# Performance work log

Measured on AMD Instinct MI355X. Metric: run time of the kernel, lower is better.

Reference implementation:

```python
import jax, jax.numpy as jnp
import numpy as np

NUM_HEADS = 8  # matches init_kwargs

def setup_inputs() -> dict:
    key = jax.random.key(0)
    ks = jax.random.split(key, 5)
    b, n, c = 8, 4096, 512
    scale_in = 1.0 / np.sqrt(c)
    return {
        'x': jax.random.normal(ks[0], (b, n, c), jnp.float32),
        'wqkv_w': jax.random.normal(ks[1], (3 * c, c), jnp.float32) * scale_in,
        'wqkv_b': jax.random.normal(ks[2], (3 * c,), jnp.float32) * 0.02,
        'wp_w': jax.random.normal(ks[3], (c, c), jnp.float32) * scale_in,
        'wp_b': jax.random.normal(ks[4], (c,), jnp.float32) * 0.02,
    }

def reference(x, wqkv_w, wqkv_b, wp_w, wp_b):
    b, n, c = x.shape
    h = NUM_HEADS
    d = c // h
    # QKV projection (torch Linear: x @ W^T + b)
    qkv = x @ wqkv_w.T + wqkv_b                      # (b, n, 3c)
    qkv = jnp.transpose(qkv.reshape(b, n, 3, c), (2, 0, 1, 3))
    q, k, v = qkv[0], qkv[1], qkv[2]                 # each (b, n, c)
    # Faithful to original: reshape (b,n,h,d) -> (b,h,n,d) is a FLAT
    # reinterpretation (torch .reshape), not a transpose.
    q = q.reshape(b, n, h, d).reshape(b, h, n, d)
    k = k.reshape(b, n, h, d).reshape(b, h, n, d)
    v = v.reshape(b, n, h, d).reshape(b, h, n, d)
    # Channel (cross-covariance) attention: contract over tokens n.
    scores = jnp.einsum('bhnd,bhne->bhde', q, k) / jnp.sqrt(jnp.float32(d))
    weights = jax.nn.softmax(scores, axis=-1)        # softmax over head_dim
    y = jnp.einsum('bhde,bhme->bhdm', weights, v)    # (b, h, d, n)
    y = jnp.transpose(y, (0, 3, 1, 2)).reshape(b, n, c)
    return y @ wp_w.T + wp_b
```

## Files before the change

kernel.cpp:

```cpp
#include <hip/hip_runtime.h>

typedef short s16x8 __attribute__((ext_vector_type(8)));
typedef float f32x4 __attribute__((ext_vector_type(4)));
typedef unsigned short us;

__device__ inline us f2bf(float f){
    union{float f;unsigned u;} v{f};
    unsigned r = v.u + 0x7fff + ((v.u>>16)&1);
    return (us)(r>>16);
}

__device__ __forceinline__ void glds16(const us* g, us* l){
    __builtin_amdgcn_global_load_lds(
        (const __attribute__((address_space(1))) unsigned int*)(g),
        (__attribute__((address_space(3))) unsigned int*)(l), 16, 0, 0);
}

__global__ void cast_all(const float* __restrict__ x, const float* __restrict__ wqkv_w,
                         const float* __restrict__ wp_w, us* __restrict__ xbf,
                         us* __restrict__ wqkvbf, us* __restrict__ wpbf){
    int i = blockIdx.x*blockDim.x + threadIdx.x;
    const float* s; us* d; int j;
    if(i < 4194304){ s = x; d = xbf; j = i; }
    else if(i < 4390912){ s = wqkv_w; d = wqkvbf; j = i - 4194304; }
    else { s = wp_w; d = wpbf; j = i - 4390912; }
    float4 f = ((const float4*)s)[j];
    ushort4 o;
    o.x = f2bf(f.x); o.y = f2bf(f.y); o.z = f2bf(f.z); o.w = f2bf(f.w);
    ((ushort4*)d)[j] = o;
}

__launch_bounds__(256,4)
__global__ void gemm_qkv(const us* __restrict__ A, const us* __restrict__ B,
                         const float* __restrict__ bias, us* __restrict__ C){
    __shared__ __attribute__((aligned(16))) us sA[128*64];
    __shared__ __attribute__((aligned(16))) us sB[128*64];
    int t = threadIdx.x;
    int id = blockIdx.x;
    int xcd = id & 7, s = id >> 3;
    int nt = s % 12, mt = xcd*32 + s/12;
    int lane = t&63, wave = t>>6, quad = lane>>4, l15 = lane&15;
    int wm = wave>>1, wn = wave&1;

    int l8 = lane>>3;
    int sw = ((lane&7) ^ l8)*8;
    const us* Ag = A + (size_t)(mt*128 + wave*32 + l8)*512 + sw;
    const us* Bg = B + (size_t)(nt*128 + wave*32 + l8)*512 + sw;
    us* sAw = &sA[(wave*32)*64];
    us* sBw = &sB[(wave*32)*64];

    f32x4 acc[4][4];
    #pragma unroll
    for(int i=0;i<4;i++)
        #pragma unroll
        for(int j=0;j<4;j++) acc[i][j] = (f32x4){0.f,0.f,0.f,0.f};

    for(int k0=0; k0<512; k0+=64){
        glds16(Ag + k0,           sAw);
        glds16(Ag + 8*512 + k0,   sAw + 8*64);
        glds16(Ag + 16*512 + k0,  sAw + 16*64);
        glds16(Ag + 24*512 + k0,  sAw + 24*64);
        glds16(Bg + k0,           sBw);
        glds16(Bg + 8*512 + k0,   sBw + 8*64);
        glds16(Bg + 16*512 + k0,  sBw + 16*64);
        glds16(Bg + 24*512 + k0,  sBw + 24*64);
        __syncthreads();
        #pragma unroll
        for(int ks=0; ks<2; ks++){
            int kc = ks*4 + quad;
            s16x8 af[4], bfr[4];
            #pragma unroll
            for(int i=0;i<4;i++){
                int r = wm*64 + i*16 + l15;
                af[i] = *(const s16x8*)&sA[r*64 + ((kc ^ (r&7))<<3)];
            }
            #pragma unroll
            for(int j=0;j<4;j++){
                int r = wn*64 + j*16 + l15;
                bfr[j] = *(const s16x8*)&sB[r*64 + ((kc ^ (r&7))<<3)];
            }
            #pragma unroll
            for(int i=0;i<4;i++)
                #pragma unroll
                for(int j=0;j<4;j++)
                    acc[i][j] = __builtin_amdgcn_mfma_f32_16x16x32_bf16(af[i], bfr[j], acc[i][j], 0,0,0);
        }
        __syncthreads();
    }

    int row0 = mt*128 + wm*64, col0 = nt*128 + wn*64;
    #pragma unroll
    for(int j=0;j<4;j++){
        int col = col0 + j*16 + l15;
        float bv = bias[col];
        #pragma unroll
        for(int i=0;i<4;i++){
            int rbase = row0 + i*16 + quad*4;
            #pragma unroll
            for(int r=0;r<4;r++)
                C[(size_t)(rbase+r)*1536 + col] = f2bf(acc[i][j][r] + bv);
        }
    }
}

__launch_bounds__(256,4)
__global__ void attn_scores_mfma(const us* __restrict__ qkv, float* __restrict__ Sp){
    __shared__ __attribute__((aligned(16))) us sQt[64*72];
    __shared__ __attribute__((aligned(16))) us sKt[64*72];
    int t = threadIdx.x;
    int kb = blockIdx.x, head = blockIdx.y;
    int lane = t & 63, w = t >> 6;
    int quad = lane >> 4, l15 = lane & 15;
    int p = t & 31;
    int d0 = (t >> 5) * 8;

    f32x4 acc[4];
    #pragma unroll
    for(int j=0;j<4;j++) acc[j] = (f32x4){0.f,0.f,0.f,0.f};

    for(int chunk=0; chunk<8; chunk++){
        int r0 = head*512 + kb*64 + chunk*8;
        const us* g = qkv + (size_t)(r0 + (p>>2))*1536 + (2*(p&3))*64 + d0;
        union{uint4 v; us h[8];} q0, q1, k0, k1;
        q0.v = *(const uint4*)g;         q1.v = *(const uint4*)(g + 64);
        k0.v = *(const uint4*)(g + 512); k1.v = *(const uint4*)(g + 576);
        #pragma unroll
        for(int j=0;j<8;j++){
            *(unsigned*)&sQt[(d0+j)*72 + 2*p] = (unsigned)q0.h[j] | ((unsigned)q1.h[j]<<16);
            *(unsigned*)&sKt[(d0+j)*72 + 2*p] = (unsigned)k0.h[j] | ((unsigned)k1.h[j]<<16);
        }
        __syncthreads();
        int d = w*16 + l15;
        #pragma unroll
        for(int ks=0; ks<2; ks++){
            int tb = ks*4 + quad;
            s16x8 af = *(const s16x8*)&sQt[d*72 + tb*8];
            #pragma unroll
            for(int jt=0; jt<4; jt++){
                int e = jt*16 + l15;
                s16x8 bfv = *(const s16x8*)&sKt[e*72 + tb*8];
                acc[jt] = __builtin_amdgcn_mfma_f32_16x16x32_bf16(af, bfv, acc[jt], 0,0,0);
            }
        }
        __syncthreads();
    }

    float* S = Sp + (size_t)(kb*64 + head)*4096;
    #pragma unroll
    for(int jt=0; jt<4; jt++){
        int e = jt*16 + l15;
        #pragma unroll
        for(int r=0; r<4; r++){
            int d = w*16 + quad*4 + r;
            S[d*64 + e] = acc[jt][r];
        }
    }
}

__global__ void softmax64(const float* __restrict__ Sp, us* __restrict__ W){
    int head = blockIdx.x>>2, part = blockIdx.x&3;
    int t = threadIdx.x;
    int d = part*16 + (t>>4), e0 = (t&15)*4;
    float4 v = {0.f,0.f,0.f,0.f};
    for(int kb=0; kb<8; kb++){
        float4 f = *(const float4*)&Sp[(size_t)(kb*64 + head)*4096 + d*64 + e0];
        v.x+=f.x; v.y+=f.y; v.z+=f.z; v.w+=f.w;
    }
    v.x*=0.125f; v.y*=0.125f; v.z*=0.125f; v.w*=0.125f;
    float m = fmaxf(fmaxf(v.x,v.y), fmaxf(v.z,v.w));
    m = fmaxf(m, __shfl_xor(m, 1));
    m = fmaxf(m, __shfl_xor(m, 2));
    m = fmaxf(m, __shfl_xor(m, 4));
    m = fmaxf(m, __shfl_xor(m, 8));
    v.x=__expf(v.x-m); v.y=__expf(v.y-m); v.z=__expf(v.z-m); v.w=__expf(v.w-m);
    float s = v.x+v.y+v.z+v.w;
    s += __shfl_xor(s, 1);
    s += __shfl_xor(s, 2);
    s += __shfl_xor(s, 4);
    s += __shfl_xor(s, 8);
    float inv = 1.f/s;
    union{uint2 u; us h[4];} o;
    o.h[0]=f2bf(v.x*inv); o.h[1]=f2bf(v.y*inv); o.h[2]=f2bf(v.z*inv); o.h[3]=f2bf(v.w*inv);
    *(uint2*)&W[(size_t)head*4096 + d*64 + e0] = o.u;
}

__launch_bounds__(256,2)
__global__ void fold(const us* __restrict__ Wsm, const us* __restrict__ wpbf,
                     us* __restrict__ Mcat){
    __shared__ us sWt[64*72];
    int t = threadIdx.x;
    int head = blockIdx.x>>2, part = blockIdx.x&3;
    int b = head>>3, h = head&7;
    int lane = t&63, w = t>>6, quad = lane>>4, l15 = lane&15;
    #pragma unroll
    for(int it=0; it<2; it++){
        int idx = it*2048 + t*8;
        int d = idx>>6, e0 = idx&63;
        union{uint4 v; us s[8];} q;
        q.v = *(const uint4*)&Wsm[(size_t)head*4096 + idx];
        #pragma unroll
        for(int j=0;j<8;j++) sWt[(e0+j)*72 + d] = q.s[j];
    }
    __syncthreads();
    #pragma unroll
    for(int i=0;i<2;i++){
        int nO = part*128 + w*32 + i*16 + l15;
        s16x8 af0 = *(const s16x8*)&wpbf[(size_t)nO*512 + h*64 + quad*8];
        s16x8 af1 = *(const s16x8*)&wpbf[(size_t)nO*512 + h*64 + 32 + quad*8];
        #pragma unroll
        for(int j=0;j<4;j++){
            s16x8 bf0 = *(const s16x8*)&sWt[(j*16+l15)*72 + quad*8];
            s16x8 bf1 = *(const s16x8*)&sWt[(j*16+l15)*72 + 32 + quad*8];
            f32x4 acc = (f32x4){0.f,0.f,0.f,0.f};
            acc = __builtin_amdgcn_mfma_f32_16x16x32_bf16(af0, bf0, acc, 0,0,0);
            acc = __builtin_amdgcn_mfma_f32_16x16x32_bf16(af1, bf1, acc, 0,0,0);
            #pragma unroll
            for(int r=0;r<4;r++){
                int row = part*128 + w*32 + i*16 + quad*4 + r;
                Mcat[((size_t)(b*512 + row))*512 + h*64 + j*16 + l15] = f2bf(acc[r]);
            }
        }
    }
}

__launch_bounds__(256,4)
__global__ void gemm_vout(const us* __restrict__ qkv, const us* __restrict__ Mcat,
                          const float* __restrict__ bias, float* __restrict__ out){
    __shared__ __attribute__((aligned(16))) us sA[128*64];
    __shared__ __attribute__((aligned(16))) us sB[128*64];
    int t = threadIdx.x;
    int id = blockIdx.x;
    int xcd = id & 7, s = id >> 3;
    int nt = s & 3, mt = xcd*32 + (s>>2);
    int b = mt>>5, mr = mt&31;
    int lane = t&63, wave = t>>6, quad = lane>>4, l15 = lane&15;
    int wm = wave>>1, wn = wave&1;

    int l8 = lane>>3;
    int sw = ((lane&7) ^ l8)*8;
    const us* Abase = qkv + ((size_t)(8*b)*512 + mr*16 + wave*4)*1536 + 1024 + l8*64 + sw;
    const us* Bbase = Mcat + ((size_t)(b*512 + nt*128 + wave*32 + l8))*512 + sw;
    us* sAw = &sA[(wave*32)*64];
    us* sBw = &sB[(wave*32)*64];

    f32x4 acc[4][4];
    #pragma unroll
    for(int i=0;i<4;i++)
        #pragma unroll
        for(int j=0;j<4;j++) acc[i][j] = (f32x4){0.f,0.f,0.f,0.f};

    for(int h=0; h<8; h++){
        const us* Ah = Abase + (size_t)h*512*1536;
        const us* Bh = Bbase + h*64;
        glds16(Ah,           sAw);
        glds16(Ah + 1536,    sAw + 8*64);
        glds16(Ah + 2*1536,  sAw + 16*64);
        glds16(Ah + 3*1536,  sAw + 24*64);
        glds16(Bh,           sBw);
        glds16(Bh + 8*512,   sBw + 8*64);
        glds16(Bh + 16*512,  sBw + 16*64);
        glds16(Bh + 24*512,  sBw + 24*64);
        __syncthreads();
        #pragma unroll
        for(int ks=0; ks<2; ks++){
            int kc = ks*4 + quad;
            s16x8 af[4], bfr[4];
            #pragma unroll
            for(int i=0;i<4;i++){
                int r = wm*64 + i*16 + l15;
                af[i] = *(const s16x8*)&sA[r*64 + ((kc ^ (r&7))<<3)];
            }
            #pragma unroll
            for(int j=0;j<4;j++){
                int r = wn*64 + j*16 + l15;
                bfr[j] = *(const s16x8*)&sB[r*64 + ((kc ^ (r&7))<<3)];
            }
            #pragma unroll
            for(int i=0;i<4;i++)
                #pragma unroll
                for(int j=0;j<4;j++)
                    acc[i][j] = __builtin_amdgcn_mfma_f32_16x16x32_bf16(af[i], bfr[j], acc[i][j], 0,0,0);
        }
        __syncthreads();
    }

    int row0 = b*4096 + mr*128 + wm*64;
    int col0 = nt*128 + wn*64;
    #pragma unroll
    for(int j=0;j<4;j++){
        int col = col0 + j*16 + l15;
        float bv = bias[col];
        #pragma unroll
        for(int i=0;i<4;i++){
            int rbase = row0 + i*16 + quad*4;
            #pragma unroll
            for(int r2=0;r2<4;r2++)
                out[(size_t)(rbase+r2)*512 + col] = acc[i][j][r2] + bv;
        }
    }
}

extern "C" void kernel_launch(void* const* d_in, const int* in_sizes, int n_in,
                              void* d_out, int out_size, void* d_ws, size_t ws_size,
                              hipStream_t stream){
    const float* x      = (const float*)d_in[0];
    const float* wqkv_w = (const float*)d_in[1];
    const float* wqkv_b = (const float*)d_in[2];
    const float* wp_w   = (const float*)d_in[3];
    const float* wp_b   = (const float*)d_in[4];

    char* ws = (char*)d_ws;
    us*    qkvbf  = (us*)(ws);
    us*    xbf    = (us*)(ws + 100663296);
    float* Spart  = (float*)(ws + 134217728);
    us*    Wsm    = (us*)(ws + 142606336);
    us*    Mcat   = (us*)(ws + 143130624);
    us*    wqkvbf = (us*)(ws + 147324928);
    us*    wpbf   = (us*)(ws + 148897792);

    cast_all<<<17408,256,0,stream>>>(x, wqkv_w, wp_w, xbf, wqkvbf, wpbf);

    gemm_qkv<<<3072,256,0,stream>>>(xbf, wqkvbf, wqkv_b, qkvbf);

    attn_scores_mfma<<<dim3(8,64),256,0,stream>>>(qkvbf, Spart);
    softmax64<<<256,256,0,stream>>>(Spart, Wsm);
    fold<<<256,256,0,stream>>>(Wsm, wpbf, Mcat);

    gemm_vout<<<1024,256,0,stream>>>(qkvbf, Mcat, wp_b, (float*)d_out);
}
```

Baseline: 233.3 us.

## Double-buffer GEMMs with 256x256 tiles, 8 waves, and MFMA priority scheduling

```diff
diff --git a/kernel.cpp b/kernel.cpp
--- a/kernel.cpp
+++ b/kernel.cpp
@@ -30,75 +30,103 @@
     ((ushort4*)d)[j] = o;
 }
 
-__launch_bounds__(256,4)
+__launch_bounds__(512,2)
 __global__ void gemm_qkv(const us* __restrict__ A, const us* __restrict__ B,
                          const float* __restrict__ bias, us* __restrict__ C){
-    __shared__ __attribute__((aligned(16))) us sA[128*64];
-    __shared__ __attribute__((aligned(16))) us sB[128*64];
+    __shared__ __attribute__((aligned(16))) us sA[2][16384];
+    __shared__ __attribute__((aligned(16))) us sB[2][16384];
     int t = threadIdx.x;
     int id = blockIdx.x;
     int xcd = id & 7, s = id >> 3;
-    int nt = s % 12, mt = xcd*32 + s/12;
+    int nt = s % 6, mt = xcd*16 + s/6;
     int lane = t&63, wave = t>>6, quad = lane>>4, l15 = lane&15;
-    int wm = wave>>1, wn = wave&1;
-
+    int wm = wave>>2, wn = wave&3;
     int l8 = lane>>3;
     int sw = ((lane&7) ^ l8)*8;
-    const us* Ag = A + (size_t)(mt*128 + wave*32 + l8)*512 + sw;
-    const us* Bg = B + (size_t)(nt*128 + wave*32 + l8)*512 + sw;
-    us* sAw = &sA[(wave*32)*64];
-    us* sBw = &sB[(wave*32)*64];
-
-    f32x4 acc[4][4];
-    #pragma unroll
-    for(int i=0;i<4;i++)
-        #pragma unroll
-        for(int j=0;j<4;j++) acc[i][j] = (f32x4){0.f,0.f,0.f,0.f};
-
-    for(int k0=0; k0<512; k0+=64){
-        glds16(Ag + k0,           sAw);
-        glds16(Ag + 8*512 + k0,   sAw + 8*64);
-        glds16(Ag + 16*512 + k0,  sAw + 16*64);
-        glds16(Ag + 24*512 + k0,  sAw + 24*64);
-        glds16(Bg + k0,           sBw);
-        glds16(Bg + 8*512 + k0,   sBw + 8*64);
-        glds16(Bg + 16*512 + k0,  sBw + 16*64);
-        glds16(Bg + 24*512 + k0,  sBw + 24*64);
-        __syncthreads();
-        #pragma unroll
-        for(int ks=0; ks<2; ks++){
-            int kc = ks*4 + quad;
-            s16x8 af[4], bfr[4];
-            #pragma unroll
-            for(int i=0;i<4;i++){
-                int r = wm*64 + i*16 + l15;
-                af[i] = *(const s16x8*)&sA[r*64 + ((kc ^ (r&7))<<3)];
-            }
-            #pragma unroll
-            for(int j=0;j<4;j++){
-                int r = wn*64 + j*16 + l15;
-                bfr[j] = *(const s16x8*)&sB[r*64 + ((kc ^ (r&7))<<3)];
-            }
-            #pragma unroll
-            for(int i=0;i<4;i++)
+
+    const us* Ag = A + (size_t)(mt*256 + wave*8 + l8)*512 + sw;
+    const us* Bg = B + (size_t)(nt*256 + wave*8 + l8)*512 + sw;
+    us* sA0 = &sA[0][0];
+    us* sB0 = &sB[0][0];
+    int wofs = wave*512;
+
+    f32x4 acc[8][4];
+    #pragma unroll
+    for(int m=0;m<8;m++)
+        #pragma unroll
+        for(int n=0;n<4;n++) acc[m][n] = (f32x4){0.f,0.f,0.f,0.f};
+
+    #pragma unroll
+    for(int r=0;r<4;r++) glds16(Ag + r*32768, sA0 + wofs + r*4096);
+    #pragma unroll
+    for(int r=0;r<4;r++) glds16(Bg + r*32768, sB0 + wofs + r*4096);
+    asm volatile("s_waitcnt vmcnt(0)" ::: "memory");
+    __builtin_amdgcn_s_barrier();
+
+    for(int kt=0; kt<8; ++kt){
+        int cur = kt & 1;
+        const us* sAc = sA0 + cur*16384;
+        const us* sBc = sB0 + cur*16384;
+        if(kt < 7){
+            int kn = (kt+1)*64;
+            int nx = (cur^1)*16384 + wofs;
+            #pragma unroll
+            for(int r=0;r<4;r++) glds16(Ag + r*32768 + kn, sA0 + nx + r*4096);
+            #pragma unroll
+            for(int r=0;r<4;r++) glds16(Bg + r*32768 + kn, sB0 + nx + r*4096);
+        }
+        s16x8 bfr[4][2];
+        #pragma unroll
+        for(int n=0;n<4;n++){
+            int rw = wn*64 + n*16 + l15;
+            #pragma unroll
+            for(int ks=0;ks<2;ks++){
+                int kc = ks*4 + quad;
+                bfr[n][ks] = *(const s16x8*)&sBc[rw*64 + ((kc ^ (rw&7))<<3)];
+            }
+        }
+        #pragma unroll
+        for(int p=0;p<4;p++){
+            s16x8 af[2][2];
+            #pragma unroll
+            for(int i=0;i<2;i++){
+                int rw = wm*128 + (2*p+i)*16 + l15;
                 #pragma unroll
-                for(int j=0;j<4;j++)
-                    acc[i][j] = __builtin_amdgcn_mfma_f32_16x16x32_bf16(af[i], bfr[j], acc[i][j], 0,0,0);
-        }
-        __syncthreads();
-    }
-
-    int row0 = mt*128 + wm*64, col0 = nt*128 + wn*64;
-    #pragma unroll
-    for(int j=0;j<4;j++){
-        int col = col0 + j*16 + l15;
+                for(int ks=0;ks<2;ks++){
+                    int kc = ks*4 + quad;
+                    af[i][ks] = *(const s16x8*)&sAc[rw*64 + ((kc ^ (rw&7))<<3)];
+                }
+            }
+            __builtin_amdgcn_s_barrier();
+            __builtin_amdgcn_s_setprio(1);
+            #pragma unroll
+            for(int ks=0;ks<2;ks++)
+                #pragma unroll
+                for(int i=0;i<2;i++)
+                    #pragma unroll
+                    for(int n=0;n<4;n++)
+                        acc[2*p+i][n] = __builtin_amdgcn_mfma_f32_16x16x32_bf16(
+                                            af[i][ks], bfr[n][ks], acc[2*p+i][n], 0,0,0);
+            __builtin_amdgcn_s_setprio(0);
+            __builtin_amdgcn_s_barrier();
+        }
+        if(kt < 7){
+            asm volatile("s_waitcnt vmcnt(0)" ::: "memory");
+            __builtin_amdgcn_s_barrier();
+        }
+    }
+
+    int row0 = mt*256 + wm*128, col0 = nt*256 + wn*64;
+    #pragma unroll
+    for(int n=0;n<4;n++){
+        int col = col0 + n*16 + l15;
         float bv = bias[col];
         #pragma unroll
-        for(int i=0;i<4;i++){
-            int rbase = row0 + i*16 + quad*4;
+        for(int m=0;m<8;m++){
+            int rb = row0 + m*16 + quad*4;
             #pragma unroll
             for(int r=0;r<4;r++)
-                C[(size_t)(rbase+r)*1536 + col] = f2bf(acc[i][j][r] + bv);
+                C[(size_t)(rb+r)*1536 + col] = f2bf(acc[m][n][r] + bv);
         }
     }
 }
@@ -223,79 +251,106 @@
     }
 }
 
-__launch_bounds__(256,4)
+__launch_bounds__(512,2)
 __global__ void gemm_vout(const us* __restrict__ qkv, const us* __restrict__ Mcat,
                           const float* __restrict__ bias, float* __restrict__ out){
-    __shared__ __attribute__((aligned(16))) us sA[128*64];
-    __shared__ __attribute__((aligned(16))) us sB[128*64];
+    __shared__ __attribute__((aligned(16))) us sA[2][16384];
+    __shared__ __attribute__((aligned(16))) us sB[2][16384];
     int t = threadIdx.x;
     int id = blockIdx.x;
     int xcd = id & 7, s = id >> 3;
-    int nt = s & 3, mt = xcd*32 + (s>>2);
-    int b = mt>>5, mr = mt&31;
+    int f = xcd*32 + s;
+    int b = f>>5, rr = f&31, mtb = rr>>1, nt = rr&1;
     int lane = t&63, wave = t>>6, quad = lane>>4, l15 = lane&15;
-    int wm = wave>>1, wn = wave&1;
-
+    int wm = wave>>2, wn = wave&3;
     int l8 = lane>>3;
     int sw = ((lane&7) ^ l8)*8;
-    const us* Abase = qkv + ((size_t)(8*b)*512 + mr*16 + wave*4)*1536 + 1024 + l8*64 + sw;
-    const us* Bbase = Mcat + ((size_t)(b*512 + nt*128 + wave*32 + l8))*512 + sw;
-    us* sAw = &sA[(wave*32)*64];
-    us* sBw = &sB[(wave*32)*64];
-
-    f32x4 acc[4][4];
-    #pragma unroll
-    for(int i=0;i<4;i++)
-        #pragma unroll
-        for(int j=0;j<4;j++) acc[i][j] = (f32x4){0.f,0.f,0.f,0.f};
-
-    for(int h=0; h<8; h++){
-        const us* Ah = Abase + (size_t)h*512*1536;
-        const us* Bh = Bbase + h*64;
-        glds16(Ah,           sAw);
-        glds16(Ah + 1536,    sAw + 8*64);
-        glds16(Ah + 2*1536,  sAw + 16*64);
-        glds16(Ah + 3*1536,  sAw + 24*64);
-        glds16(Bh,           sBw);
-        glds16(Bh + 8*512,   sBw + 8*64);
-        glds16(Bh + 16*512,  sBw + 16*64);
-        glds16(Bh + 24*512,  sBw + 24*64);
-        __syncthreads();
-        #pragma unroll
-        for(int ks=0; ks<2; ks++){
-            int kc = ks*4 + quad;
-            s16x8 af[4], bfr[4];
-            #pragma unroll
-            for(int i=0;i<4;i++){
-                int r = wm*64 + i*16 + l15;
-                af[i] = *(const s16x8*)&sA[r*64 + ((kc ^ (r&7))<<3)];
-            }
-            #pragma unroll
-            for(int j=0;j<4;j++){
-                int r = wn*64 + j*16 + l15;
-                bfr[j] = *(const s16x8*)&sB[r*64 + ((kc ^ (r&7))<<3)];
-            }
-            #pragma unroll
-            for(int i=0;i<4;i++)
+
+    const us* Ag = qkv + (size_t)(b*4096 + mtb*32 + wave)*1536 + 1024 + l8*64 + sw;
+    const us* Bg = Mcat + (size_t)(b*512 + nt*256 + wave*8 + l8)*512 + sw;
+    us* sA0 = &sA[0][0];
+    us* sB0 = &sB[0][0];
+    int wofs = wave*512;
+
+    f32x4 acc[8][4];
+    #pragma unroll
+    for(int m=0;m<8;m++)
+        #pragma unroll
+        for(int n=0;n<4;n++) acc[m][n] = (f32x4){0.f,0.f,0.f,0.f};
+
+    #pragma unroll
+    for(int r=0;r<4;r++) glds16(Ag + r*12288, sA0 + wofs + r*4096);
+    #pragma unroll
+    for(int r=0;r<4;r++) glds16(Bg + r*32768, sB0 + wofs + r*4096);
+    asm volatile("s_waitcnt vmcnt(0)" ::: "memory");
+    __builtin_amdgcn_s_barrier();
+
+    for(int kt=0; kt<8; ++kt){
+        int cur = kt & 1;
+        const us* sAc = sA0 + cur*16384;
+        const us* sBc = sB0 + cur*16384;
+        if(kt < 7){
+            int nx = (cur^1)*16384 + wofs;
+            size_t ka = (size_t)(kt+1)*786432;
+            int kb2 = (kt+1)*64;
+            #pragma unroll
+            for(int r=0;r<4;r++) glds16(Ag + ka + r*12288, sA0 + nx + r*4096);
+            #pragma unroll
+            for(int r=0;r<4;r++) glds16(Bg + kb2 + r*32768, sB0 + nx + r*4096);
+        }
+        s16x8 bfr[4][2];
+        #pragma unroll
+        for(int n=0;n<4;n++){
+            int rw = wn*64 + n*16 + l15;
+            #pragma unroll
+            for(int ks=0;ks<2;ks++){
+                int kc = ks*4 + quad;
+                bfr[n][ks] = *(const s16x8*)&sBc[rw*64 + ((kc ^ (rw&7))<<3)];
+            }
+        }
+        #pragma unroll
+        for(int p=0;p<4;p++){
+            s16x8 af[2][2];
+            #pragma unroll
+            for(int i=0;i<2;i++){
+                int rw = wm*128 + (2*p+i)*16 + l15;
                 #pragma unroll
-                for(int j=0;j<4;j++)
-                    acc[i][j] = __builtin_amdgcn_mfma_f32_16x16x32_bf16(af[i], bfr[j], acc[i][j], 0,0,0);
-        }
-        __syncthreads();
-    }
-
-    int row0 = b*4096 + mr*128 + wm*64;
-    int col0 = nt*128 + wn*64;
-    #pragma unroll
-    for(int j=0;j<4;j++){
-        int col = col0 + j*16 + l15;
+                for(int ks=0;ks<2;ks++){
+                    int kc = ks*4 + quad;
+                    af[i][ks] = *(const s16x8*)&sAc[rw*64 + ((kc ^ (rw&7))<<3)];
+                }
+            }
+            __builtin_amdgcn_s_barrier();
+            __builtin_amdgcn_s_setprio(1);
+            #pragma unroll
+            for(int ks=0;ks<2;ks++)
+                #pragma unroll
+                for(int i=0;i<2;i++)
+                    #pragma unroll
+                    for(int n=0;n<4;n++)
+                        acc[2*p+i][n] = __builtin_amdgcn_mfma_f32_16x16x32_bf16(
+                                            af[i][ks], bfr[n][ks], acc[2*p+i][n], 0,0,0);
+            __builtin_amdgcn_s_setprio(0);
+            __builtin_amdgcn_s_barrier();
+        }
+        if(kt < 7){
+            asm volatile("s_waitcnt vmcnt(0)" ::: "memory");
+            __builtin_amdgcn_s_barrier();
+        }
+    }
+
+    int row0 = b*4096 + mtb*256 + wm*128;
+    int col0 = nt*256 + wn*64;
+    #pragma unroll
+    for(int n=0;n<4;n++){
+        int col = col0 + n*16 + l15;
         float bv = bias[col];
         #pragma unroll
-        for(int i=0;i<4;i++){
-            int rbase = row0 + i*16 + quad*4;
+        for(int m=0;m<8;m++){
+            int rb = row0 + m*16 + quad*4;
             #pragma unroll
             for(int r2=0;r2<4;r2++)
-                out[(size_t)(rbase+r2)*512 + col] = acc[i][j][r2] + bv;
+                out[(size_t)(rb+r2)*512 + col] = acc[m][n][r2] + bv;
         }
     }
 }
@@ -320,11 +375,11 @@
 
     cast_all<<<17408,256,0,stream>>>(x, wqkv_w, wp_w, xbf, wqkvbf, wpbf);
 
-    gemm_qkv<<<3072,256,0,stream>>>(xbf, wqkvbf, wqkv_b, qkvbf);
+    gemm_qkv<<<768,512,0,stream>>>(xbf, wqkvbf, wqkv_b, qkvbf);
 
     attn_scores_mfma<<<dim3(8,64),256,0,stream>>>(qkvbf, Spart);
     softmax64<<<256,256,0,stream>>>(Spart, Wsm);
     fold<<<256,256,0,stream>>>(Wsm, wpbf, Mcat);
 
-    gemm_vout<<<1024,256,0,stream>>>(qkvbf, Mcat, wp_b, (float*)d_out);
-}
+    gemm_vout<<<256,512,0,stream>>>(qkvbf, Mcat, wp_b, (float*)d_out);
+}
```

New measurement: 262.6 us. 12.6% more time.

## Restructure QKV GEMM into 256x256 double-buffered tiles with interleaved prefetch

Applied to the files above, without the earlier changes.

```diff
diff --git a/kernel.cpp b/kernel.cpp
--- a/kernel.cpp
+++ b/kernel.cpp
@@ -30,75 +30,159 @@
     ((ushort4*)d)[j] = o;
 }
 
-__launch_bounds__(256,4)
+__launch_bounds__(512,2)
 __global__ void gemm_qkv(const us* __restrict__ A, const us* __restrict__ B,
                          const float* __restrict__ bias, us* __restrict__ C){
-    __shared__ __attribute__((aligned(16))) us sA[128*64];
-    __shared__ __attribute__((aligned(16))) us sB[128*64];
+    __shared__ __attribute__((aligned(16))) us sA[2][16384];
+    __shared__ __attribute__((aligned(16))) us sB[2][16384];
     int t = threadIdx.x;
     int id = blockIdx.x;
     int xcd = id & 7, s = id >> 3;
-    int nt = s % 12, mt = xcd*32 + s/12;
-    int lane = t&63, wave = t>>6, quad = lane>>4, l15 = lane&15;
-    int wm = wave>>1, wn = wave&1;
-
+    int nt = s % 6, mt = xcd*16 + s/6;
+    int lane = t&63, w = t>>6, quad = lane>>4, l15 = lane&15;
+    int wm = w>>2, wn = w&3;
     int l8 = lane>>3;
     int sw = ((lane&7) ^ l8)*8;
-    const us* Ag = A + (size_t)(mt*128 + wave*32 + l8)*512 + sw;
-    const us* Bg = B + (size_t)(nt*128 + wave*32 + l8)*512 + sw;
-    us* sAw = &sA[(wave*32)*64];
-    us* sBw = &sB[(wave*32)*64];
-
-    f32x4 acc[4][4];
-    #pragma unroll
-    for(int i=0;i<4;i++)
-        #pragma unroll
-        for(int j=0;j<4;j++) acc[i][j] = (f32x4){0.f,0.f,0.f,0.f};
-
-    for(int k0=0; k0<512; k0+=64){
-        glds16(Ag + k0,           sAw);
-        glds16(Ag + 8*512 + k0,   sAw + 8*64);
-        glds16(Ag + 16*512 + k0,  sAw + 16*64);
-        glds16(Ag + 24*512 + k0,  sAw + 24*64);
-        glds16(Bg + k0,           sBw);
-        glds16(Bg + 8*512 + k0,   sBw + 8*64);
-        glds16(Bg + 16*512 + k0,  sBw + 16*64);
-        glds16(Bg + 24*512 + k0,  sBw + 24*64);
-        __syncthreads();
-        #pragma unroll
-        for(int ks=0; ks<2; ks++){
-            int kc = ks*4 + quad;
-            s16x8 af[4], bfr[4];
-            #pragma unroll
-            for(int i=0;i<4;i++){
-                int r = wm*64 + i*16 + l15;
-                af[i] = *(const s16x8*)&sA[r*64 + ((kc ^ (r&7))<<3)];
-            }
-            #pragma unroll
-            for(int j=0;j<4;j++){
-                int r = wn*64 + j*16 + l15;
-                bfr[j] = *(const s16x8*)&sB[r*64 + ((kc ^ (r&7))<<3)];
-            }
+
+    int rA0 = wm*128 + (w&3)*8;
+    int rB0 = (w>>1)*64 + (w&1)*8;
+    const us* Ag = A + (size_t)(mt*256 + rA0 + l8)*512 + sw;
+    const us* Bg = B + (size_t)(nt*256 + rB0 + l8)*512 + sw;
+    us* sA0 = &sA[0][0];
+    us* sB0 = &sB[0][0];
+    int aofs = rA0*64, bofs = rB0*64;
+
+#define STA(r,kt,bo) glds16(Ag + (size_t)(r)*16384 + (size_t)(kt)*64, sA0 + (bo) + aofs + (r)*2048)
+#define STB(r,kt,bo) glds16(Bg + (size_t)(r)*8192  + (size_t)(kt)*64, sB0 + (bo) + bofs + (r)*1024)
+
+    f32x4 acc[8][4];
+    #pragma unroll
+    for(int m=0;m<8;m++)
+        #pragma unroll
+        for(int n=0;n<4;n++) acc[m][n] = (f32x4){0.f,0.f,0.f,0.f};
+
+    STA(0,0,0); STA(1,0,0); STB(0,0,0); STB(1,0,0);
+    STB(2,0,0); STB(3,0,0); STA(2,0,0); STA(3,0,0);
+    asm volatile("s_waitcnt vmcnt(4)" ::: "memory");
+    __builtin_amdgcn_s_barrier();
+
+    s16x8 aF[4][2], bF[4][2];
+    for(int kt=0; kt<8; ++kt){
+        int co = (kt&1)*16384, no = co^16384;
+        const us* sAc = sA0 + co;
+        const us* sBc = sB0 + co;
+
+        #pragma unroll
+        for(int i=0;i<4;i++){
+            int rw = wm*128 + i*16 + l15;
+            #pragma unroll
+            for(int ks=0;ks<2;ks++){
+                int kc = ks*4 + quad;
+                aF[i][ks] = *(const s16x8*)&sAc[rw*64 + ((kc ^ (rw&7))<<3)];
+            }
+        }
+        #pragma unroll
+        for(int n=0;n<2;n++){
+            int rw = wn*64 + n*16 + l15;
+            #pragma unroll
+            for(int ks=0;ks<2;ks++){
+                int kc = ks*4 + quad;
+                bF[n][ks] = *(const s16x8*)&sBc[rw*64 + ((kc ^ (rw&7))<<3)];
+            }
+        }
+        if(kt<7){ STA(0,kt+1,no); STA(1,kt+1,no);
+                  asm volatile("s_waitcnt vmcnt(4)" ::: "memory"); }
+        else    { asm volatile("s_waitcnt vmcnt(2)" ::: "memory"); }
+        __builtin_amdgcn_s_barrier();
+        __builtin_amdgcn_s_setprio(1);
+        #pragma unroll
+        for(int ks=0;ks<2;ks++)
             #pragma unroll
             for(int i=0;i<4;i++)
                 #pragma unroll
-                for(int j=0;j<4;j++)
-                    acc[i][j] = __builtin_amdgcn_mfma_f32_16x16x32_bf16(af[i], bfr[j], acc[i][j], 0,0,0);
-        }
-        __syncthreads();
-    }
-
-    int row0 = mt*128 + wm*64, col0 = nt*128 + wn*64;
-    #pragma unroll
-    for(int j=0;j<4;j++){
-        int col = col0 + j*16 + l15;
-        float bv = bias[col];
+                for(int n=0;n<2;n++)
+                    acc[i][n] = __builtin_amdgcn_mfma_f32_16x16x32_bf16(bF[n][ks], aF[i][ks], acc[i][n], 0,0,0);
+        __builtin_amdgcn_s_setprio(0);
+        __builtin_amdgcn_s_barrier();
+
+        #pragma unroll
+        for(int n=2;n<4;n++){
+            int rw = wn*64 + n*16 + l15;
+            #pragma unroll
+            for(int ks=0;ks<2;ks++){
+                int kc = ks*4 + quad;
+                bF[n][ks] = *(const s16x8*)&sBc[rw*64 + ((kc ^ (rw&7))<<3)];
+            }
+        }
+        if(kt<7){ STB(0,kt+1,no); STB(1,kt+1,no);
+                  asm volatile("s_waitcnt vmcnt(4)" ::: "memory"); }
+        else    { asm volatile("s_waitcnt vmcnt(0)" ::: "memory"); }
+        __builtin_amdgcn_s_barrier();
+        __builtin_amdgcn_s_setprio(1);
+        #pragma unroll
+        for(int ks=0;ks<2;ks++)
+            #pragma unroll
+            for(int i=0;i<4;i++)
+                #pragma unroll
+                for(int n=2;n<4;n++)
+                    acc[i][n] = __builtin_amdgcn_mfma_f32_16x16x32_bf16(bF[n][ks], aF[i][ks], acc[i][n], 0,0,0);
+        __builtin_amdgcn_s_setprio(0);
+        __builtin_amdgcn_s_barrier();
+
         #pragma unroll
         for(int i=0;i<4;i++){
-            int rbase = row0 + i*16 + quad*4;
-            #pragma unroll
-            for(int r=0;r<4;r++)
-                C[(size_t)(rbase+r)*1536 + col] = f2bf(acc[i][j][r] + bv);
+            int rw = wm*128 + (4+i)*16 + l15;
+            #pragma unroll
+            for(int ks=0;ks<2;ks++){
+                int kc = ks*4 + quad;
+                aF[i][ks] = *(const s16x8*)&sAc[rw*64 + ((kc ^ (rw&7))<<3)];
+            }
+        }
+        if(kt<7){ STB(2,kt+1,no); STB(3,kt+1,no); }
+        __builtin_amdgcn_s_barrier();
+        __builtin_amdgcn_s_setprio(1);
+        #pragma unroll
+        for(int ks=0;ks<2;ks++)
+            #pragma unroll
+            for(int i=0;i<4;i++)
+                #pragma unroll
+                for(int n=0;n<2;n++)
+                    acc[4+i][n] = __builtin_amdgcn_mfma_f32_16x16x32_bf16(bF[n][ks], aF[i][ks], acc[4+i][n], 0,0,0);
+        __builtin_amdgcn_s_setprio(0);
+        __builtin_amdgcn_s_barrier();
+
+        if(kt<7){ STA(2,kt+1,no); STA(3,kt+1,no);
+                  asm volatile("s_waitcnt vmcnt(4)" ::: "memory"); }
+        __builtin_amdgcn_s_barrier();
+        __builtin_amdgcn_s_setprio(1);
+        #pragma unroll
+        for(int ks=0;ks<2;ks++)
+            #pragma unroll
+            for(int i=0;i<4;i++)
+                #pragma unroll
+                for(int n=2;n<4;n++)
+                    acc[4+i][n] = __builtin_amdgcn_mfma_f32_16x16x32_bf16(bF[n][ks], aF[i][ks], acc[4+i][n], 0,0,0);
+        __builtin_amdgcn_s_setprio(0);
+        __builtin_amdgcn_s_barrier();
+    }
+#undef STA
+#undef STB
+
+    int row0 = mt*256 + wm*128, col0 = nt*256 + wn*64;
+    float4 bv[4];
+    #pragma unroll
+    for(int n=0;n<4;n++) bv[n] = *(const float4*)&bias[col0 + n*16 + quad*4];
+    #pragma unroll
+    for(int m=0;m<8;m++){
+        size_t rb = (size_t)(row0 + m*16 + l15)*1536 + col0;
+        #pragma unroll
+        for(int n=0;n<4;n++){
+            ushort4 o;
+            o.x = f2bf(acc[m][n][0] + bv[n].x);
+            o.y = f2bf(acc[m][n][1] + bv[n].y);
+            o.z = f2bf(acc[m][n][2] + bv[n].z);
+            o.w = f2bf(acc[m][n][3] + bv[n].w);
+            *(ushort4*)&C[rb + n*16 + quad*4] = o;
         }
     }
 }
@@ -320,7 +404,7 @@
 
     cast_all<<<17408,256,0,stream>>>(x, wqkv_w, wp_w, xbf, wqkvbf, wpbf);
 
-    gemm_qkv<<<3072,256,0,stream>>>(xbf, wqkvbf, wqkv_b, qkvbf);
+    gemm_qkv<<<768,512,0,stream>>>(xbf, wqkvbf, wqkv_b, qkvbf);
 
     attn_scores_mfma<<<dim3(8,64),256,0,stream>>>(qkvbf, Spart);
     softmax64<<<256,256,0,stream>>>(Spart, Wsm);
```

Result: slower. 256.5 us (+10.0%).

## Vectorize GEMM epilogue stores via swapped MFMA operands; double-buffer scores LDS

Applied to the files above, without the earlier changes.

```diff
diff --git a/kernel.cpp b/kernel.cpp
--- a/kernel.cpp
+++ b/kernel.cpp
@@ -83,30 +83,34 @@
             for(int i=0;i<4;i++)
                 #pragma unroll
                 for(int j=0;j<4;j++)
-                    acc[i][j] = __builtin_amdgcn_mfma_f32_16x16x32_bf16(af[i], bfr[j], acc[i][j], 0,0,0);
+                    acc[i][j] = __builtin_amdgcn_mfma_f32_16x16x32_bf16(bfr[j], af[i], acc[i][j], 0,0,0);
         }
         __syncthreads();
     }
 
     int row0 = mt*128 + wm*64, col0 = nt*128 + wn*64;
-    #pragma unroll
-    for(int j=0;j<4;j++){
-        int col = col0 + j*16 + l15;
-        float bv = bias[col];
-        #pragma unroll
-        for(int i=0;i<4;i++){
-            int rbase = row0 + i*16 + quad*4;
-            #pragma unroll
-            for(int r=0;r<4;r++)
-                C[(size_t)(rbase+r)*1536 + col] = f2bf(acc[i][j][r] + bv);
+    float4 bv[4];
+    #pragma unroll
+    for(int j=0;j<4;j++) bv[j] = *(const float4*)&bias[col0 + j*16 + quad*4];
+    #pragma unroll
+    for(int i=0;i<4;i++){
+        size_t rb = (size_t)(row0 + i*16 + l15)*1536 + col0;
+        #pragma unroll
+        for(int j=0;j<4;j++){
+            ushort4 o;
+            o.x = f2bf(acc[i][j][0] + bv[j].x);
+            o.y = f2bf(acc[i][j][1] + bv[j].y);
+            o.z = f2bf(acc[i][j][2] + bv[j].z);
+            o.w = f2bf(acc[i][j][3] + bv[j].w);
+            *(ushort4*)&C[rb + j*16 + quad*4] = o;
         }
     }
 }
 
 __launch_bounds__(256,4)
 __global__ void attn_scores_mfma(const us* __restrict__ qkv, float* __restrict__ Sp){
-    __shared__ __attribute__((aligned(16))) us sQt[64*72];
-    __shared__ __attribute__((aligned(16))) us sKt[64*72];
+    __shared__ __attribute__((aligned(16))) us sQt[2][64*72];
+    __shared__ __attribute__((aligned(16))) us sKt[2][64*72];
     int t = threadIdx.x;
     int kb = blockIdx.x, head = blockIdx.y;
     int lane = t & 63, w = t >> 6;
@@ -118,28 +122,44 @@
     #pragma unroll
     for(int j=0;j<4;j++) acc[j] = (f32x4){0.f,0.f,0.f,0.f};
 
-    for(int chunk=0; chunk<8; chunk++){
-        int r0 = head*512 + kb*64 + chunk*8;
-        const us* g = qkv + (size_t)(r0 + (p>>2))*1536 + (2*(p&3))*64 + d0;
-        union{uint4 v; us h[8];} q0, q1, k0, k1;
-        q0.v = *(const uint4*)g;         q1.v = *(const uint4*)(g + 64);
-        k0.v = *(const uint4*)(g + 512); k1.v = *(const uint4*)(g + 576);
-        #pragma unroll
-        for(int j=0;j<8;j++){
-            *(unsigned*)&sQt[(d0+j)*72 + 2*p] = (unsigned)q0.h[j] | ((unsigned)q1.h[j]<<16);
-            *(unsigned*)&sKt[(d0+j)*72 + 2*p] = (unsigned)k0.h[j] | ((unsigned)k1.h[j]<<16);
-        }
-        __syncthreads();
+    const us* gbase = qkv + (size_t)(head*512 + kb*64 + (p>>2))*1536 + (2*(p&3))*64 + d0;
+    union U{uint4 v; us h[8];};
+    U q0,q1,k0,k1;
+    q0.v = *(const uint4*)gbase;         q1.v = *(const uint4*)(gbase + 64);
+    k0.v = *(const uint4*)(gbase + 512); k1.v = *(const uint4*)(gbase + 576);
+    #pragma unroll
+    for(int j=0;j<8;j++){
+        *(unsigned*)&sQt[0][(d0+j)*72 + 2*p] = (unsigned)q0.h[j] | ((unsigned)q1.h[j]<<16);
+        *(unsigned*)&sKt[0][(d0+j)*72 + 2*p] = (unsigned)k0.h[j] | ((unsigned)k1.h[j]<<16);
+    }
+    __syncthreads();
+
+    #pragma unroll
+    for(int c=0; c<8; c++){
+        if(c<7){
+            const us* g = gbase + (size_t)(c+1)*8*1536;
+            q0.v = *(const uint4*)g;         q1.v = *(const uint4*)(g + 64);
+            k0.v = *(const uint4*)(g + 512); k1.v = *(const uint4*)(g + 576);
+        }
+        const us* Q = sQt[c&1];
+        const us* K = sKt[c&1];
         int d = w*16 + l15;
         #pragma unroll
         for(int ks=0; ks<2; ks++){
             int tb = ks*4 + quad;
-            s16x8 af = *(const s16x8*)&sQt[d*72 + tb*8];
+            s16x8 af = *(const s16x8*)&Q[d*72 + tb*8];
             #pragma unroll
             for(int jt=0; jt<4; jt++){
-                int e = jt*16 + l15;
-                s16x8 bfv = *(const s16x8*)&sKt[e*72 + tb*8];
+                s16x8 bfv = *(const s16x8*)&K[(jt*16+l15)*72 + tb*8];
                 acc[jt] = __builtin_amdgcn_mfma_f32_16x16x32_bf16(af, bfv, acc[jt], 0,0,0);
+            }
+        }
+        if(c<7){
+            int nb = (c+1)&1;
+            #pragma unroll
+            for(int j=0;j<8;j++){
+                *(unsigned*)&sQt[nb][(d0+j)*72 + 2*p] = (unsigned)q0.h[j] | ((unsigned)q1.h[j]<<16);
+                *(unsigned*)&sKt[nb][(d0+j)*72 + 2*p] = (unsigned)k0.h[j] | ((unsigned)k1.h[j]<<16);
             }
         }
         __syncthreads();
@@ -279,23 +299,27 @@
             for(int i=0;i<4;i++)
                 #pragma unroll
                 for(int j=0;j<4;j++)
-                    acc[i][j] = __builtin_amdgcn_mfma_f32_16x16x32_bf16(af[i], bfr[j], acc[i][j], 0,0,0);
+                    acc[i][j] = __builtin_amdgcn_mfma_f32_16x16x32_bf16(bfr[j], af[i], acc[i][j], 0,0,0);
         }
         __syncthreads();
     }
 
     int row0 = b*4096 + mr*128 + wm*64;
     int col0 = nt*128 + wn*64;
-    #pragma unroll
-    for(int j=0;j<4;j++){
-        int col = col0 + j*16 + l15;
-        float bv = bias[col];
-        #pragma unroll
-        for(int i=0;i<4;i++){
-            int rbase = row0 + i*16 + quad*4;
-            #pragma unroll
-            for(int r2=0;r2<4;r2++)
-                out[(size_t)(rbase+r2)*512 + col] = acc[i][j][r2] + bv;
+    float4 bv[4];
+    #pragma unroll
+    for(int j=0;j<4;j++) bv[j] = *(const float4*)&bias[col0 + j*16 + quad*4];
+    #pragma unroll
+    for(int i=0;i<4;i++){
+        size_t rb = (size_t)(row0 + i*16 + l15)*512 + col0;
+        #pragma unroll
+        for(int j=0;j<4;j++){
+            float4 o;
+            o.x = acc[i][j][0] + bv[j].x;
+            o.y = acc[i][j][1] + bv[j].y;
+            o.z = acc[i][j][2] + bv[j].z;
+            o.w = acc[i][j][3] + bv[j].w;
+            *(float4*)&out[rb + j*16 + quad*4] = o;
         }
     }
 }
```

Result: slower. 242.8 us (+4.1%).
